# Performance work log

Hardware: AMD Instinct MI355X
Metric: run time of the kernel (lower is better)

Reference implementation:

```python
import jax, jax.numpy as jnp
import numpy as np

B, T, D = 1, 4096, 2048
NUM_HEADS, NUM_KV_HEADS, HEAD_DIM = 16, 8, 128
QUERY_PRE_ATTN_SCALAR = HEAD_DIM ** -0.5
SOFT_CAP = 50.0
WINDOW = 1024
ROPE_BASE = 10000.0
ROPE_SCALE = 1.0
K_MASK = -2.3819763e+38


def apply_rope(x, positions, head_dim, max_wavelength=ROPE_BASE, scale_factor=ROPE_SCALE):
    # x: [B, T, N, H], positions: [B, T]
    fraction = 2.0 * jnp.arange(head_dim // 2, dtype=jnp.float32) / head_dim
    timescale = max_wavelength ** fraction  # [H/2]
    sinusoid = positions[..., None].astype(jnp.float32) / timescale  # [B, T, H/2]
    sinusoid = (sinusoid / scale_factor)[..., None, :]  # [B, T, 1, H/2]
    sin, cos = jnp.sin(sinusoid), jnp.cos(sinusoid)
    first, second = jnp.split(x, 2, axis=-1)
    out = jnp.concatenate([first * cos - second * sin,
                           second * cos + first * sin], axis=-1)
    return out.astype(x.dtype)


def setup_inputs() -> dict:
    key = jax.random.key(0)
    ks = jax.random.split(key, 4)
    x = jax.random.normal(ks[0], (B, T, D), dtype=jnp.float32)
    segment_pos = jnp.broadcast_to(jnp.arange(T, dtype=jnp.int32), (B, T))
    # causal mask [B, T, S]
    attn_mask = jnp.broadcast_to(
        jnp.tril(jnp.ones((T, T), dtype=jnp.bool_)), (B, T, T))
    q_w = jax.random.normal(ks[1], (NUM_HEADS, D, HEAD_DIM), dtype=jnp.float32) * 0.02
    kv_w = jax.random.normal(ks[2], (2, NUM_KV_HEADS, D, HEAD_DIM), dtype=jnp.float32) * 0.02
    o_w = jax.random.normal(ks[3], (NUM_HEADS, HEAD_DIM, D), dtype=jnp.float32) * 0.02
    return {"x": x, "segment_pos": segment_pos, "attn_mask": attn_mask,
            "q_w": q_w, "kv_w": kv_w, "o_w": o_w}


def reference(x, segment_pos, attn_mask, q_w, kv_w, o_w):
    # Projections (GQA: separate q and kv einsums)
    q = jnp.einsum('BTD,NDH->BTNH', x, q_w)          # [B,T,N,H]
    k = jnp.einsum('BSD,KDH->BSKH', x, kv_w[0])      # [B,S,K,H]
    v = jnp.einsum('BSD,KDH->BSKH', x, kv_w[1])      # [B,S,K,H]

    q = apply_rope(q, segment_pos, HEAD_DIM)
    q = q * QUERY_PRE_ATTN_SCALAR
    k = apply_rope(k, segment_pos, HEAD_DIM)

    num_groups = NUM_HEADS // NUM_KV_HEADS
    qg = q.reshape(B, T, NUM_KV_HEADS, num_groups, HEAD_DIM)
    logits = jnp.einsum('BTKGH,BSKH->BTKGS', qg, k)
    logits = logits.reshape(B, T, NUM_HEADS, -1)     # [B,T,N,S]

    # soft cap
    logits = jnp.tanh(logits / SOFT_CAP) * SOFT_CAP

    # sliding-window mask combined with causal mask
    all_ones = jnp.ones_like(attn_mask)
    sliding = jnp.triu(all_ones, -WINDOW + 1) * jnp.tril(all_ones, WINDOW - 1)
    mask = sliding * attn_mask                       # [B,T,S] bool

    padded = jnp.where(mask[:, :, None, :], logits, K_MASK)
    probs = jax.nn.softmax(padded, axis=-1).astype(k.dtype)

    probs_g = probs.reshape(B, T, NUM_KV_HEADS, num_groups, -1)
    encoded = jnp.einsum('BTKGS,BSKH->BTKGH', probs_g, v)
    encoded = encoded.reshape(B, T, NUM_HEADS, HEAD_DIM)

    attn_output = jnp.einsum('BTNH,NHD->BTD', encoded, o_w)
    return attn_output
```

## Files before the change

kernel.cpp:

```cpp
#include <hip/hip_runtime.h>
#include <hip/hip_bf16.h>
#include <math.h>

typedef __attribute__((ext_vector_type(8))) short short8;
typedef __attribute__((ext_vector_type(8))) unsigned short ushort8;
typedef __attribute__((ext_vector_type(4))) float f32x4;
typedef __attribute__((ext_vector_type(2))) float f32x2;

#define T_SEQ 4096
#define D_MODEL 2048
#define N_HEADS 16
#define N_KV 8
#define HEAD_DIM 128
#define QSCALE 0.08838834764831845f

__device__ __forceinline__ float bf2f(unsigned short u) {
  union { unsigned int i; float f; } x; x.i = ((unsigned int)u) << 16; return x.f;
}
__device__ __forceinline__ unsigned short f2bf(float f) {
  union { float f; unsigned int i; } x; x.f = f;
  unsigned int i = x.i;
  unsigned int r = i + 0x7fffu + ((i >> 16) & 1u);
  return (unsigned short)(r >> 16);
}

__global__ __launch_bounds__(256) void prep_kernel(const float* __restrict__ x,
                                                   unsigned short* __restrict__ xb,
                                                   const int* __restrict__ segpos,
                                                   float2* __restrict__ tab) {
  int b = blockIdx.x;
  if (b < 4096) {
    int idx = b * 256 + threadIdx.x;
    const float4* p = reinterpret_cast<const float4*>(x) + (size_t)idx * 2;
    float4 a = p[0], c = p[1];
    ushort8 o;
    o[0] = f2bf(a.x); o[1] = f2bf(a.y); o[2] = f2bf(a.z); o[3] = f2bf(a.w);
    o[4] = f2bf(c.x); o[5] = f2bf(c.y); o[6] = f2bf(c.z); o[7] = f2bf(c.w);
    reinterpret_cast<ushort8*>(xb)[idx] = o;
  } else {
    int idx = (b - 4096) * 256 + threadIdx.x;
    int t = idx >> 6, i = idx & 63;
    float pos = (float)segpos[t];
    float ts = powf(10000.f, (float)(2 * i) / 128.f);
    float ang = pos / ts;
    tab[idx] = make_float2(sinf(ang), cosf(ang));
  }
}

__global__ __launch_bounds__(256) void wqkv_transpose_kernel(const float* __restrict__ q_w,
                                                             const float* __restrict__ kv_w,
                                                             unsigned short* __restrict__ Wt) {
  __shared__ float tile[32][33];
  int z = blockIdx.z;
  const float* src = (z < 16) ? q_w + (size_t)z * 2048 * 128
                              : kv_w + (size_t)(z - 16) * 2048 * 128;
  unsigned short* dst = Wt + (size_t)z * 128 * 2048;
  int c0 = blockIdx.x * 32, r0 = blockIdx.y * 32;
  int tx = threadIdx.x & 31, ty = threadIdx.x >> 5;
#pragma unroll
  for (int i = 0; i < 4; ++i)
    tile[ty + i * 8][tx] = src[(size_t)(r0 + ty + i * 8) * 128 + c0 + tx];
  __syncthreads();
#pragma unroll
  for (int i = 0; i < 4; ++i)
    dst[(size_t)(c0 + ty + i * 8) * 2048 + r0 + tx] = f2bf(tile[tx][ty + i * 8]);
}

__global__ __launch_bounds__(256) void ow_transpose_kernel(const float* __restrict__ src,
                                                           unsigned short* __restrict__ dst) {
  __shared__ float tile[32][33];
  int c0 = blockIdx.x * 32, r0 = blockIdx.y * 32;
  int tx = threadIdx.x & 31, ty = threadIdx.x >> 5;
#pragma unroll
  for (int i = 0; i < 4; ++i)
    tile[ty + i * 8][tx] = src[(size_t)(r0 + ty + i * 8) * 2048 + c0 + tx];
  __syncthreads();
#pragma unroll
  for (int i = 0; i < 4; ++i)
    dst[(size_t)(c0 + ty + i * 8) * 2048 + r0 + tx] = f2bf(tile[tx][ty + i * 8]);
}

#define G2L(gp, lp)                                                           \
  __builtin_amdgcn_global_load_lds(                                           \
      (const __attribute__((address_space(1))) void*)(gp),                    \
      (__attribute__((address_space(3))) void*)(lp), 16, 0, 0)
#define GBAR() asm volatile("s_barrier" ::: "memory")
#define VMW(n) asm volatile("s_waitcnt vmcnt(" #n ")" ::: "memory")
#define LGKM0()                                                               \
  { asm volatile("s_waitcnt lgkmcnt(0)" ::: "memory");                        \
    __builtin_amdgcn_sched_barrier(0); }

template <int OUT_BF16, int MHB>
__global__ __launch_bounds__(512, 2) void gemm256_kernel(const unsigned short* __restrict__ A,
                                                         const unsigned short* __restrict__ Bt,
                                                         void* __restrict__ Cout,
                                                         int M, int N, int K) {
  extern __shared__ unsigned short smem[];
  unsigned short* ldsA = smem;
  unsigned short* ldsB = smem + 2 * MHB * 8192;
  const int tid = threadIdx.x;
  const int lane = tid & 63, wave = tid >> 6;
  const int wm = wave >> 2, wn = wave & 3;
  const int lr = lane & 15, lg = lane >> 4;
  const int swz = (lr & 7) << 3;
  const int c0s = (lg * 8) ^ swz;
  const int c1s = (32 + lg * 8) ^ swz;

  int id = blockIdx.y * gridDim.x + blockIdx.x;
  int nb = gridDim.x * gridDim.y;
  int sw = (id & 7) * (nb >> 3) + (id >> 3);
  const long brow = (long)(sw / gridDim.x) * (128 * MHB);
  const long bcol = (long)(sw % gridDim.x) * 256;

  const unsigned short* Ag = A + brow * K;
  const unsigned short* Bg = Bt + bcol * K;

  const int r0 = tid >> 3;
  const int cs = ((tid & 7) * 8) ^ ((r0 & 7) << 3);

#define ST_A(tt, b, a)                                                        \
  { G2L(Ag + (size_t)((a) * 128 + r0) * K + (size_t)(tt) * 64 + cs,           \
        ldsA + (b) * (MHB * 8192) + (a) * 8192 + tid * 8);                    \
    G2L(Ag + (size_t)((a) * 128 + r0 + 64) * K + (size_t)(tt) * 64 + cs,      \
        ldsA + (b) * (MHB * 8192) + (a) * 8192 + 4096 + tid * 8); }
#define ST_B(tt, b, h)                                                        \
  { G2L(Bg + (size_t)((h) * 128 + r0) * K + (size_t)(tt) * 64 + cs,           \
        ldsB + (b) * 16384 + (h) * 8192 + tid * 8);                           \
    G2L(Bg + (size_t)((h) * 128 + r0 + 64) * K + (size_t)(tt) * 64 + cs,      \
        ldsB + (b) * 16384 + (h) * 8192 + 4096 + tid * 8); }

  f32x4 acc[4 * MHB][4] = {};
  short8 bf[4][2];
  short8 af[4];

#define RD_B(b)                                                               \
  { const unsigned short* pb = ldsB + (b) * 16384 + wn * 4096;                \
    _Pragma("unroll")                                                         \
    for (int n = 0; n < 4; ++n) {                                             \
      bf[n][0] = *(const short8*)(pb + (n * 16 + lr) * 64 + c0s);             \
      bf[n][1] = *(const short8*)(pb + (n * 16 + lr) * 64 + c1s);             \
    } }
#define RD_A(b, mb)                                                           \
  { const unsigned short* pa = ldsA + (b) * (MHB * 8192) + wm * (MHB * 4096); \
    af[0] = *(const short8*)(pa + ((mb) * 16 + lr) * 64 + c0s);               \
    af[1] = *(const short8*)(pa + ((mb) * 16 + lr) * 64 + c1s);               \
    af[2] = *(const short8*)(pa + ((mb) * 16 + 16 + lr) * 64 + c0s);          \
    af[3] = *(const short8*)(pa + ((mb) * 16 + 16 + lr) * 64 + c1s); }
#define MFMA2(mb)                                                             \
  { __builtin_amdgcn_s_setprio(1);                                            \
    _Pragma("unroll")                                                         \
    for (int n = 0; n < 4; ++n) {                                             \
      acc[mb][n]     = __builtin_amdgcn_mfma_f32_16x16x32_bf16(af[0], bf[n][0], acc[mb][n], 0, 0, 0);     \
      acc[mb][n]     = __builtin_amdgcn_mfma_f32_16x16x32_bf16(af[1], bf[n][1], acc[mb][n], 0, 0, 0);     \
      acc[mb + 1][n] = __builtin_amdgcn_mfma_f32_16x16x32_bf16(af[2], bf[n][0], acc[mb + 1][n], 0, 0, 0); \
      acc[mb + 1][n] = __builtin_amdgcn_mfma_f32_16x16x32_bf16(af[3], bf[n][1], acc[mb + 1][n], 0, 0, 0); \
    }                                                                         \
    __builtin_amdgcn_s_setprio(0); }

  ST_B(0, 0, 0); ST_B(0, 0, 1);
  ST_A(0, 0, 0);
  if constexpr (MHB == 2) ST_A(0, 0, 1);
  ST_B(1, 1, 0); ST_B(1, 1, 1);
  if constexpr (MHB == 2) { VMW(4); } else { VMW(4); }
  ST_A(1, 1, 0);
  if constexpr (MHB == 2) ST_A(1, 1, 1);
  GBAR();

#define TILE(b, tn, sflag)                                                    \
  { RD_B(b); RD_A(b, 0);                                                      \
    LGKM0(); GBAR();                \
    if (sflag) ST_B(tn, b, 0);                 \
    MFMA2(0); GBAR();                                                         \
    if constexpr (MHB == 1) {                                                 \
      RD_A(b, 2);                                                             \
      LGKM0(); GBAR();                          \
      if (sflag) { ST_B(tn, b, 1); VMW(4); ST_A(tn, b, 0); }                  \
      else       { VMW(0); }                                                  \
      MFMA2(2); GBAR();                                                       \
    } else {                                                                  \
      RD_A(b, 2);                                                             \
      if (sflag) ST_B(tn, b, 1);         \
      GBAR(); MFMA2(2); GBAR();                                               \
      RD_A(b, 4);                                                             \
      GBAR(); MFMA2(4); GBAR();                                               \
      RD_A(b, 6);                                                             \
      LGKM0(); GBAR();                          \
      if (sflag) { VMW(4); ST_A(tn, b, 0); ST_A(tn, b, 1); }                  \
      else       { VMW(0); }                                                  \
      MFMA2(6); GBAR();                                                       \
    } }

  const int NT = K >> 6;
  for (int j = 0; j < (NT >> 1); ++j) {
    const int t2 = 2 * j + 2, t3 = 2 * j + 3;
    TILE(0, t2, (t2 < NT));
    TILE(1, t3, (t3 < NT));
  }

#undef TILE
#undef ST_A
#undef ST_B
#undef RD_A
#undef RD_B
#undef MFMA2

#pragma unroll
  for (int m = 0; m < 4 * MHB; ++m) {
#pragma unroll
    for (int i = 0; i < 4; ++i) {
      long row = brow + wm * (64 * MHB) + m * 16 + lg * 4 + i;
#pragma unroll
      for (int n = 0; n < 4; ++n) {
        long col = bcol + wn * 64 + n * 16 + lr;
        if (OUT_BF16)
          ((unsigned short*)Cout)[row * N + col] = f2bf(acc[m][n][i]);
        else
          ((float*)Cout)[row * N + col] = acc[m][n][i];
      }
    }
  }
}

__global__ __launch_bounds__(256) void rope_vt_kernel(const unsigned short* __restrict__ raw,
                                                      const float2* __restrict__ tab,
                                                      unsigned short* __restrict__ Qb,
                                                      unsigned short* __restrict__ Kb,
                                                      unsigned short* __restrict__ Vt) {
  __shared__ unsigned short tile[32][33];
  int b = blockIdx.x;
  if (b < 3072) {
    int gid = b * 256 + threadIdx.x;
    int j = gid & 7;
    int rem = gid >> 3;
    int hs = rem % 24;
    int t = rem / 24;
    int i0 = j * 8;
    float sv[8], cv[8];
    const float2* tp = tab + t * 64 + i0;
#pragma unroll
    for (int q = 0; q < 8; ++q) { float2 sc2 = tp[q]; sv[q] = sc2.x; cv[q] = sc2.y; }
    if (hs < 16) {
      const unsigned short* p = raw + (size_t)t * 4096 + hs * 128 + i0;
      ushort8 a = *(const ushort8*)p;
      ushort8 c = *(const ushort8*)(p + 64);
      ushort8 o1, o2;
#pragma unroll
      for (int q = 0; q < 8; ++q) {
        float fa = bf2f(a[q]), fb = bf2f(c[q]);
        o1[q] = f2bf((fa * cv[q] - fb * sv[q]) * QSCALE);
        o2[q] = f2bf((fb * cv[q] + fa * sv[q]) * QSCALE);
      }
      unsigned short* qp = Qb + ((size_t)hs * T_SEQ + t) * 128 + i0;
      *(ushort8*)qp = o1;
      *(ushort8*)(qp + 64) = o2;
    } else {
      int kn = hs - 16;
      const unsigned short* p = raw + (size_t)t * 4096 + 2048 + kn * 128 + i0;
      ushort8 a = *(const ushort8*)p;
      ushort8 c = *(const ushort8*)(p + 64);
      ushort8 o1, o2;
#pragma unroll
      for (int q = 0; q < 8; ++q) {
        float fa = bf2f(a[q]), fb = bf2f(c[q]);
        o1[q] = f2bf(fa * cv[q] - fb * sv[q]);
        o2[q] = f2bf(fb * cv[q] + fa * sv[q]);
      }
      unsigned short* kp = Kb + ((size_t)kn * T_SEQ + t) * 128 + i0;
      *(ushort8*)kp = o1;
      *(ushort8*)(kp + 64) = o2;
    }
  } else {
    int id = b - 3072;
    int bx = id & 3, by = (id >> 2) & 127, bz = id >> 9;
    const unsigned short* src = raw + 3072 + (size_t)bz * 128;
    unsigned short* dst = Vt + (size_t)bz * 128 * 4096;
    int c0 = bx * 32, r0 = by * 32;
    int tx = threadIdx.x & 31, ty = threadIdx.x >> 5;
#pragma unroll
    for (int i = 0; i < 4; ++i)
      tile[ty + i * 8][tx] = src[(size_t)(r0 + ty + i * 8) * 4096 + c0 + tx];
    __syncthreads();
#pragma unroll
    for (int i = 0; i < 4; ++i)
      dst[(size_t)(c0 + ty + i * 8) * 4096 + r0 + tx] = tile[tx][ty + i * 8];
  }
}

__global__ __launch_bounds__(512, 2) void attn_kernel(const unsigned short* __restrict__ Qb,
                                                      const unsigned short* __restrict__ Kb,
                                                      const unsigned short* __restrict__ Vt,
                                                      unsigned short* __restrict__ enc) {
  __shared__ unsigned short Ks[64][128];
  __shared__ unsigned short Vs[128][64];
  __shared__ unsigned short Ps[8][32][72];
  int rawb = blockIdx.x;
  int lin = (rawb & 7) * 32 + (rawb >> 3);
  const int h = lin >> 4;
  const int qb0 = (lin & 15) * 256;
  const int kvh = h >> 1;
  const int tid = threadIdx.x, lane = tid & 63, wave = tid >> 6;
  const int qw = qb0 + wave * 32;
  const int lr = lane & 15, lg = lane >> 4;
  const int sw = (lr & 7) << 3;
  const int ck0 = (lg * 8) ^ sw, ck1 = (32 + lg * 8) ^ sw;
  const int ck2 = (64 + lg * 8) ^ sw, ck3 = (96 + lg * 8) ^ sw;

  short8 aq[2][4];
#pragma unroll
  for (int g = 0; g < 2; ++g) {
    const unsigned short* qp = Qb + ((size_t)h * T_SEQ + qw + g * 16 + lr) * 128 + lg * 8;
#pragma unroll
    for (int c = 0; c < 4; ++c) aq[g][c] = *(const short8*)(qp + c * 32);
  }
  f32x4 acc[2][8] = {};
  float lsum[2] = {0.f, 0.f};

  const int s_lo = (qb0 - 1023) > 0 ? (qb0 - 1023) : 0;
  const int kb_lo = s_lo >> 6, kb_hi = (qb0 + 255) >> 6;

  const int rK = tid >> 4;
  const int cpK = (tid & 15) * 8;
  const int colK = cpK ^ ((rK & 7) << 3);
  const int rV = tid >> 3;
  const int cpV = (tid & 7) * 8;
  const int colV = cpV ^ ((rV & 7) << 3);
  const unsigned short* kgb = Kb + ((size_t)kvh * T_SEQ + rK) * 128 + colK;
  const unsigned short* vgb = Vt + ((size_t)kvh * 128 + rV) * T_SEQ + colV;

  ushort8 kr0, kr1, vr0, vr1;
  {
    const int s0g = kb_lo * 64;
    kr0 = *(const ushort8*)(kgb + (size_t)s0g * 128);
    kr1 = *(const ushort8*)(kgb + (size_t)(s0g + 32) * 128);
    vr0 = *(const ushort8*)(vgb + s0g);
    vr1 = *(const ushort8*)(vgb + (size_t)64 * T_SEQ + s0g);
  }

  const int qg0 = qw + lr, qg1 = qw + 16 + lr;
  for (int kb = kb_lo; kb <= kb_hi; ++kb) {
    const int s0g = kb * 64;
    __syncthreads();
    *(ushort8*)&Ks[rK][cpK] = kr0;
    *(ushort8*)&Ks[rK + 32][cpK] = kr1;
    *(ushort8*)&Vs[rV][cpV] = vr0;
    *(ushort8*)&Vs[rV + 64][cpV] = vr1;
    __syncthreads();
    if (kb < kb_hi) {
      const int sn = s0g + 64;
      kr0 = *(const ushort8*)(kgb + (size_t)sn * 128);
      kr1 = *(const ushort8*)(kgb + (size_t)(sn + 32) * 128);
      vr0 = *(const ushort8*)(vgb + sn);
      vr1 = *(const ushort8*)(vgb + (size_t)64 * T_SEQ + sn);
    }
    if (s0g > qw + 31 || s0g + 63 < qw - 1023) continue;
    const bool interior = (s0g + 63 <= qw) && (s0g >= qw - 992);

    f32x4 sT0[4] = {}, sT1[4] = {};
    __builtin_amdgcn_s_setprio(1);
#pragma unroll
    for (int st = 0; st < 4; ++st) {
      const unsigned short* kp = &Ks[st * 16 + lr][0];
      short8 k0 = *(const short8*)(kp + ck0);
      short8 k1 = *(const short8*)(kp + ck1);
      short8 k2 = *(const short8*)(kp + ck2);
      short8 k3 = *(const short8*)(kp + ck3);
      sT0[st] = __builtin_amdgcn_mfma_f32_16x16x32_bf16(k0, aq[0][0], sT0[st], 0, 0, 0);
      sT1[st] = __builtin_amdgcn_mfma_f32_16x16x32_bf16(k0, aq[1][0], sT1[st], 0, 0, 0);
      sT0[st] = __builtin_amdgcn_mfma_f32_16x16x32_bf16(k1, aq[0][1], sT0[st], 0, 0, 0);
      sT1[st] = __builtin_amdgcn_mfma_f32_16x16x32_bf16(k1, aq[1][1], sT1[st], 0, 0, 0);
      sT0[st] = __builtin_amdgcn_mfma_f32_16x16x32_bf16(k2, aq[0][2], sT0[st], 0, 0, 0);
      sT1[st] = __builtin_amdgcn_mfma_f32_16x16x32_bf16(k2, aq[1][2], sT1[st], 0, 0, 0);
      sT0[st] = __builtin_amdgcn_mfma_f32_16x16x32_bf16(k3, aq[0][3], sT0[st], 0, 0, 0);
      sT1[st] = __builtin_amdgcn_mfma_f32_16x16x32_bf16(k3, aq[1][3], sT1[st], 0, 0, 0);
    }
    __builtin_amdgcn_s_setprio(0);

#pragma unroll
    for (int g = 0; g < 2; ++g) {
      const f32x4* sTg = g ? sT1 : sT0;
      const int qgg = g ? qg1 : qg0;
#pragma unroll
      for (int st = 0; st < 4; ++st) {
        f32x4 svv = sTg[st];
        f32x2 sa, sb;
        sa[0] = svv[0]; sa[1] = svv[1]; sb[0] = svv[2]; sb[1] = svv[3];
        f32x2 ua = sa * sa, ub = sb * sb;
        f32x2 numa = ua * 4.0e-4f + 15.f, numb = ub * 4.0e-4f + 15.f;
        f32x2 dena = ua * 2.4e-3f + 15.f, denb = ub * 2.4e-3f + 15.f;
        f32x2 ra, rb;
        ra[0] = __builtin_amdgcn_rcpf(dena[0]); ra[1] = __builtin_amdgcn_rcpf(dena[1]);
        rb[0] = __builtin_amdgcn_rcpf(denb[0]); rb[1] = __builtin_amdgcn_rcpf(denb[1]);
        f32x2 ea = (sa * 1.44269504f) * numa * ra;
        f32x2 eb = (sb * 1.44269504f) * numb * rb;
        float e[4] = {ea[0], ea[1], eb[0], eb[1]};
        float p[4];
#pragma unroll
        for (int r = 0; r < 4; ++r) {
          if (!interior) {
            int sg = s0g + st * 16 + lg * 4 + r;
            e[r] = ((unsigned)(qgg - sg) <= 1023u) ? e[r] : -__builtin_inff();
          }
          asm("v_exp_f32 %0, %1" : "=v"(p[r]) : "v"(e[r]));
        }
        lsum[g] += (p[0] + p[1]) + (p[2] + p[3]);
        unsigned u0, u1;
        asm("v_cvt_pk_bf16_f32 %0, %1, %2" : "=v"(u0) : "v"(p[0]), "v"(p[1]));
        asm("v_cvt_pk_bf16_f32 %0, %1, %2" : "=v"(u1) : "v"(p[2]), "v"(p[3]));
        uint2 w; w.x = u0; w.y = u1;
        *(uint2*)&Ps[wave][g * 16 + lr][st * 16 + lg * 4] = w;
      }
    }
    short8 pa00 = *(const short8*)&Ps[wave][lr][lg * 8];
    short8 pa01 = *(const short8*)&Ps[wave][lr][32 + lg * 8];
    short8 pa10 = *(const short8*)&Ps[wave][16 + lr][lg * 8];
    short8 pa11 = *(const short8*)&Ps[wave][16 + lr][32 + lg * 8];
    __builtin_amdgcn_s_setprio(1);
#pragma unroll
    for (int d0 = 0; d0 < 8; ++d0) {
      const unsigned short* vp = &Vs[d0 * 16 + lr][0];
      short8 bv0 = *(const short8*)(vp + ((lg * 8) ^ sw));
      short8 bv1 = *(const short8*)(vp + ((32 + lg * 8) ^ sw));
      acc[0][d0] = __builtin_amdgcn_mfma_f32_16x16x32_bf16(pa00, bv0, acc[0][d0], 0, 0, 0);
      acc[1][d0] = __builtin_amdgcn_mfma_f32_16x16x32_bf16(pa10, bv0, acc[1][d0], 0, 0, 0);
      acc[0][d0] = __builtin_amdgcn_mfma_f32_16x16x32_bf16(pa01, bv1, acc[0][d0], 0, 0, 0);
      acc[1][d0] = __builtin_amdgcn_mfma_f32_16x16x32_bf16(pa11, bv1, acc[1][d0], 0, 0, 0);
    }
    __builtin_amdgcn_s_setprio(0);
  }

#pragma unroll
  for (int g = 0; g < 2; ++g) {
    float l = lsum[g];
    l += __shfl_xor(l, 16);
    l += __shfl_xor(l, 32);
#pragma unroll
    for (int r = 0; r < 4; ++r) {
      float lt = __shfl(l, lg * 4 + r);
      float inv = __builtin_amdgcn_rcpf(lt);
      int row = qw + g * 16 + lg * 4 + r;
      unsigned short* op = enc + (size_t)row * D_MODEL + h * 128 + lr;
#pragma unroll
      for (int d0 = 0; d0 < 8; ++d0) op[d0 * 16] = f2bf(acc[g][d0][r] * inv);
    }
  }
}

extern "C" void kernel_launch(void* const* d_in, const int* in_sizes, int n_in,
                              void* d_out, int out_size, void* d_ws, size_t ws_size,
                              hipStream_t stream) {
  const float* x = (const float*)d_in[0];
  const int* segpos = (const int*)d_in[1];
  const float* q_w = (const float*)d_in[3];
  const float* kv_w = (const float*)d_in[4];
  const float* o_w = (const float*)d_in[5];
  float* out = (float*)d_out;
  char* ws = (char*)d_ws;

  const size_t OFF_XB = 0;
  const size_t OFF_WT = OFF_XB + 16777216;
  const size_t OFF_RAW = OFF_WT + 16777216;
  const size_t OFF_KB = OFF_RAW + 33554432;
  const size_t OFF_VT = OFF_KB + 8388608;
  const size_t OFF_TAB = OFF_VT + 8388608;
  unsigned short* xb = (unsigned short*)(ws + OFF_XB);
  unsigned short* Wt = (unsigned short*)(ws + OFF_WT);
  unsigned short* raw = (unsigned short*)(ws + OFF_RAW);
  unsigned short* Kb = (unsigned short*)(ws + OFF_KB);
  unsigned short* Vt = (unsigned short*)(ws + OFF_VT);
  float2* tab = (float2*)(ws + OFF_TAB);
  unsigned short* o_wt = xb;
  unsigned short* Qb = Wt;
  unsigned short* enc = raw;

  hipFuncSetAttribute((const void*)(gemm256_kernel<1, 2>),
                      hipFuncAttributeMaxDynamicSharedMemorySize, 131072);
  hipFuncSetAttribute((const void*)(gemm256_kernel<0, 1>),
                      hipFuncAttributeMaxDynamicSharedMemorySize, 98304);

  prep_kernel<<<dim3(5120), dim3(256), 0, stream>>>(x, xb, segpos, tab);
  wqkv_transpose_kernel<<<dim3(4, 64, 32), dim3(256), 0, stream>>>(q_w, kv_w, Wt);
  gemm256_kernel<1, 2><<<dim3(16, 16), dim3(512), 131072, stream>>>(xb, Wt, (void*)raw, 4096, 4096, 2048);
  ow_transpose_kernel<<<dim3(64, 64), dim3(256), 0, stream>>>(o_w, o_wt);
  rope_vt_kernel<<<dim3(7168), dim3(256), 0, stream>>>(raw, tab, Qb, Kb, Vt);
  attn_kernel<<<dim3(256), dim3(512), 0, stream>>>(Qb, Kb, Vt, enc);
  gemm256_kernel<0, 1><<<dim3(8, 32), dim3(512), 98304, stream>>>(enc, o_wt, (void*)out, 4096, 2048, 2048);
}
```

Before: 202.7 us.

## Restructure GEMM main loop to interleave A/B prefetch across sub-tiles

The macro-based TILE loop is replaced by explicit per-MHB pipelines. A-tile loads for the current buffer are deferred and interleaved with MFMA phases, and B prefetches for the next tiles are spread across sub-steps, with a barrier and lgkmcnt wait before every MFMA group. The goal is to spread global-to-LDS traffic more evenly across the MFMA work and to hide load latency. It adds more barriers per tile, and the buffer ownership ordering is changed, which risks races if the waits are off.

```diff
diff --git a/kernel.cpp b/kernel.cpp
--- a/kernel.cpp
+++ b/kernel.cpp
@@ -86,7 +86,7 @@
       (__attribute__((address_space(3))) void*)(lp), 16, 0, 0)
 #define GBAR() asm volatile("s_barrier" ::: "memory")
 #define VMW(n) asm volatile("s_waitcnt vmcnt(" #n ")" ::: "memory")
-#define LGKM0()                                                               \
+#define LG0()                                                                 \
   { asm volatile("s_waitcnt lgkmcnt(0)" ::: "memory");                        \
     __builtin_amdgcn_sched_barrier(0); }
 
@@ -157,47 +157,61 @@
     }                                                                         \
     __builtin_amdgcn_s_setprio(0); }
 
-  ST_B(0, 0, 0); ST_B(0, 0, 1);
-  ST_A(0, 0, 0);
-  if constexpr (MHB == 2) ST_A(0, 0, 1);
-  ST_B(1, 1, 0); ST_B(1, 1, 1);
-  if constexpr (MHB == 2) { VMW(4); } else { VMW(4); }
-  ST_A(1, 1, 0);
-  if constexpr (MHB == 2) ST_A(1, 1, 1);
-  GBAR();
-
-#define TILE(b, tn, sflag)                                                    \
-  { RD_B(b); RD_A(b, 0);                                                      \
-    LGKM0(); GBAR();                \
-    if (sflag) ST_B(tn, b, 0);                 \
-    MFMA2(0); GBAR();                                                         \
-    if constexpr (MHB == 1) {                                                 \
-      RD_A(b, 2);                                                             \
-      LGKM0(); GBAR();                          \
-      if (sflag) { ST_B(tn, b, 1); VMW(4); ST_A(tn, b, 0); }                  \
-      else       { VMW(0); }                                                  \
-      MFMA2(2); GBAR();                                                       \
-    } else {                                                                  \
-      RD_A(b, 2);                                                             \
-      if (sflag) ST_B(tn, b, 1);         \
-      GBAR(); MFMA2(2); GBAR();                                               \
-      RD_A(b, 4);                                                             \
-      GBAR(); MFMA2(4); GBAR();                                               \
-      RD_A(b, 6);                                                             \
-      LGKM0(); GBAR();                          \
-      if (sflag) { VMW(4); ST_A(tn, b, 0); ST_A(tn, b, 1); }                  \
-      else       { VMW(0); }                                                  \
-      MFMA2(6); GBAR();                                                       \
-    } }
-
   const int NT = K >> 6;
-  for (int j = 0; j < (NT >> 1); ++j) {
-    const int t2 = 2 * j + 2, t3 = 2 * j + 3;
-    TILE(0, t2, (t2 < NT));
-    TILE(1, t3, (t3 < NT));
-  }
-
-#undef TILE
+
+  if constexpr (MHB == 2) {
+    ST_B(0, 0, 0); ST_B(0, 0, 1); ST_A(0, 0, 0); ST_A(0, 0, 1);
+    ST_B(1, 1, 0); ST_B(1, 1, 1);
+    VMW(4); GBAR();
+    for (int j = 0; j < (NT >> 1); ++j) {
+      const int c1 = 2 * j + 1, t2 = 2 * j + 2, t3 = 2 * j + 3;
+      const bool s2 = t2 < NT, s3 = t3 < NT;
+      RD_B(0); RD_A(0, 0); ST_A(c1, 1, 0);
+      GBAR(); LG0(); MFMA2(0); GBAR();
+      RD_A(0, 2); ST_A(c1, 1, 1);
+      if (s2) ST_B(t2, 0, 0);
+      GBAR(); LG0(); MFMA2(2); GBAR();
+      RD_A(0, 4);
+      if (s2) ST_B(t2, 0, 1);
+      GBAR(); LG0(); MFMA2(4); GBAR();
+      RD_A(0, 6);
+      if (s2) { VMW(4); } else { VMW(0); }
+      GBAR(); LG0(); MFMA2(6); GBAR();
+      RD_B(1); RD_A(1, 0);
+      if (s2) ST_A(t2, 0, 0);
+      GBAR(); LG0(); MFMA2(0); GBAR();
+      RD_A(1, 2);
+      if (s2) ST_A(t2, 0, 1);
+      if (s3) ST_B(t3, 1, 0);
+      GBAR(); LG0(); MFMA2(2); GBAR();
+      RD_A(1, 4);
+      if (s3) ST_B(t3, 1, 1);
+      GBAR(); LG0(); MFMA2(4); GBAR();
+      RD_A(1, 6);
+      if (s3) { VMW(4); } else { VMW(0); }
+      GBAR(); LG0(); MFMA2(6); GBAR();
+    }
+  } else {
+    ST_B(0, 0, 0); ST_B(0, 0, 1); ST_A(0, 0, 0);
+    ST_B(1, 1, 0); ST_B(1, 1, 1);
+    VMW(4); GBAR();
+    for (int j = 0; j < (NT >> 1); ++j) {
+      const int c1 = 2 * j + 1, t2 = 2 * j + 2, t3 = 2 * j + 3;
+      const bool s2 = t2 < NT, s3 = t3 < NT;
+      RD_B(0); RD_A(0, 0); ST_A(c1, 1, 0);
+      GBAR(); LG0(); MFMA2(0); GBAR();
+      RD_A(0, 2);
+      if (s2) { ST_B(t2, 0, 0); ST_B(t2, 0, 1); VMW(4); } else { VMW(0); }
+      GBAR(); LG0(); MFMA2(2); GBAR();
+      RD_B(1); RD_A(1, 0);
+      if (s2) ST_A(t2, 0, 0);
+      GBAR(); LG0(); MFMA2(0); GBAR();
+      RD_A(1, 2);
+      if (s3) { ST_B(t3, 1, 0); ST_B(t3, 1, 1); VMW(4); } else { VMW(0); }
+      GBAR(); LG0(); MFMA2(2); GBAR();
+    }
+  }
+
 #undef ST_A
 #undef ST_B
 #undef RD_A
```

Result: no change. 200.7 us (-1.0%).
